# Kernel tuning notes

Hardware: AMD Instinct MI355X
Metric: run time of the kernel (lower is better)

The kernel has to match this reference:

```python
import jax, jax.numpy as jnp
import numpy as np

B, L, T = 128, 512, 25
DHID, DFRAME, DEMB, V = 1024, 512, 128, 512
DIN = DHID + DFRAME + DEMB  # 1664, LSTMCell input
EPS = 1e-5


def setup_inputs() -> dict:
    key = jax.random.key(0)
    ks = iter(jax.random.split(key, 32))
    nk = lambda: next(ks)
    rnd = lambda shape, s=0.02: jax.random.normal(nk(), shape, jnp.float32) * s
    inp = {
        "enc": jax.random.normal(nk(), (B, L, DHID), jnp.float32),
        "frames": jax.random.normal(nk(), (B, T, 512, 7, 7), jnp.float32),
        "h0": jnp.zeros((B, DHID), jnp.float32),
        "c0": jnp.zeros((B, DHID), jnp.float32),
        "max_decode": 25,
        # learned params
        "emb_w": rnd((V, DEMB), 0.1),
        "go": jax.random.uniform(nk(), (DEMB,), jnp.float32, -0.1, 0.1),
        "conv1_w": rnd((256, 512)),  # 1x1 conv == channel matmul
        "conv1_b": jnp.zeros((256,), jnp.float32),
        "bn1_g": jnp.ones((256,), jnp.float32), "bn1_b": jnp.zeros((256,), jnp.float32),
        "bn1_m": rnd((256,), 0.1), "bn1_v": jax.random.uniform(nk(), (256,), jnp.float32, 0.5, 1.5),
        "conv2_w": rnd((64, 256)),
        "conv2_b": jnp.zeros((64,), jnp.float32),
        "bn2_g": jnp.ones((64,), jnp.float32), "bn2_b": jnp.zeros((64,), jnp.float32),
        "bn2_m": rnd((64,), 0.1), "bn2_v": jax.random.uniform(nk(), (64,), jnp.float32, 0.5, 1.5),
        "fc_w": rnd((DFRAME, 64 * 7 * 7)), "fc_b": jnp.zeros((DFRAME,), jnp.float32),
        "hfc_w": rnd((DHID, DHID)), "hfc_b": jnp.zeros((DHID,), jnp.float32),
        "w_ih": rnd((4 * DHID, DIN)), "b_ih": jnp.zeros((4 * DHID,), jnp.float32),
        "w_hh": rnd((4 * DHID, DHID)), "b_hh": jnp.zeros((4 * DHID,), jnp.float32),
        "actor_w": rnd((DEMB, DHID + DIN)), "actor_b": jnp.zeros((DEMB,), jnp.float32),
    }
    return inp


def _decode(enc, frames, h0, c0, emb_w, go, conv1_w, conv1_b, bn1_g, bn1_b, bn1_m, bn1_v,
            conv2_w, conv2_b, bn2_g, bn2_b, bn2_m, bn2_v, fc_w, fc_b, hfc_w, hfc_b,
            w_ih, b_ih, w_hh, b_hh, actor_w, actor_b, max_t):
    b = enc.shape[0]
    sh = lambda p: p.reshape(1, -1, 1, 1)

    def bn(x, g, bb, m, v):  # eval-mode batchnorm, x: [B,C,7,7]
        return sh(g) * (x - sh(m)) * jax.lax.rsqrt(sh(v) + EPS) + sh(bb)

    def vis(x):  # ResnetVisualEncoder, x: [B,512,7,7]
        x = jnp.einsum('bchw,oc->bohw', x, conv1_w) + sh(conv1_b)
        x = jax.nn.relu(bn(x, bn1_g, bn1_b, bn1_m, bn1_v))
        x = jnp.einsum('bchw,oc->bohw', x, conv2_w) + sh(conv2_b)
        x = jax.nn.relu(bn(x, bn2_g, bn2_b, bn2_m, bn2_v))
        return x.reshape(b, -1) @ fc_w.T + fc_b  # [B, dframe]

    def step(carry, frame_t):
        h, c, e = carry
        vis_t = vis(frame_t)
        q = h @ hfc_w.T + hfc_b                          # h_tm1_fc
        raw = jnp.einsum('bld,bd->bl', enc, q)           # inp.bmm(h)
        score = jax.nn.softmax(raw, axis=1)              # over L
        weighted = jnp.einsum('bl,bld->bd', score, enc)  # DotAttn output
        inp = jnp.concatenate([vis_t, weighted, e], axis=1)  # [B, din]
        gates = inp @ w_ih.T + b_ih + h @ w_hh.T + b_hh
        i, f, g, o = jnp.split(gates, 4, axis=1)
        c_t = jax.nn.sigmoid(f) * c + jax.nn.sigmoid(i) * jnp.tanh(g)
        h_t = jax.nn.sigmoid(o) * jnp.tanh(c_t)
        cont = jnp.concatenate([h_t, inp], axis=1)
        action_emb = cont @ actor_w.T + actor_b
        action = action_emb @ emb_w.T                    # [B, V]
        e_t = emb_w[jnp.argmax(action, axis=1)]          # greedy feedback (eval)
        return (h_t, c_t, e_t), (action, score[..., None])

    e0 = jnp.broadcast_to(go, (b, go.shape[0]))
    frames_tbchw = jnp.swapaxes(frames[:, :max_t], 0, 1)  # [T,B,512,7,7]
    (h_t, c_t, _), (actions, scores) = jax.lax.scan(step, (h0, c0, e0), frames_tbchw)
    # out_action_high [B,T,V], out_attn_scores [B,T,L,1], state_t
    return jnp.swapaxes(actions, 0, 1), jnp.swapaxes(scores, 0, 1), h_t, c_t


def reference(enc, frames, h0, c0, max_decode, emb_w, go, conv1_w, conv1_b, bn1_g, bn1_b,
              bn1_m, bn1_v, conv2_w, conv2_b, bn2_g, bn2_b, bn2_m, bn2_v, fc_w, fc_b,
              hfc_w, hfc_b, w_ih, b_ih, w_hh, b_hh, actor_w, actor_b):
    max_t = min(int(max_decode), frames.shape[1])
    return _decode(enc, frames, h0, c0, emb_w, go, conv1_w, conv1_b, bn1_g, bn1_b, bn1_m,
                   bn1_v, conv2_w, conv2_b, bn2_g, bn2_b, bn2_m, bn2_v, fc_w, fc_b,
                   hfc_w, hfc_b, w_ih, b_ih, w_hh, b_hh, actor_w, actor_b, max_t)
```

## Files before the change

### kernel.cpp

```cpp
#include <hip/hip_runtime.h>
#include <cmath>


#define NB   128
#define NT   25
#define NL   512
#define DH   1024
#define DF   512
#define DE   128
#define DIN  1664
#define DCAT 2688
#define NV   512
#define NSEG 8
#define NGZ  6

#define ACT_OFF 0
#define SC_OFF  1638400
#define H_OFF   3276800
#define C_OFF   3407872

#define WS_W1T   0u
#define WS_W2T   131072u
#define WS_APT   147456u
#define WS_EWT   491520u
#define WS_BSUM  557056u
#define WS_A1    561152u
#define WS_B1    561408u
#define WS_A2    561664u
#define WS_B2    561728u
#define WS_XCAT  561792u
#define WS_CBUF  905856u
#define WS_QPART 1036928u
#define WS_VIS   4776576u
#define WS_Y2F   6414976u
#define WS_ATT   6414976u
#define WS_ATTRAW 7471744u
#define WS_GPART 7537280u

__global__ __launch_bounds__(256) void k_prep(
    const float* __restrict__ conv1_w, const float* __restrict__ conv1_b,
    const float* __restrict__ bn1_g, const float* __restrict__ bn1_b,
    const float* __restrict__ bn1_m, const float* __restrict__ bn1_v,
    const float* __restrict__ conv2_w, const float* __restrict__ conv2_b,
    const float* __restrict__ bn2_g, const float* __restrict__ bn2_b,
    const float* __restrict__ bn2_m, const float* __restrict__ bn2_v,
    const float* __restrict__ actor_w, const float* __restrict__ emb_w,
    const float* __restrict__ b_ih, const float* __restrict__ b_hh,
    float* __restrict__ ws)
{
  int i = blockIdx.x * 256 + threadIdx.x;
  if (i < 131072) {
    int c = i >> 8, o = i & 255;
    ws[WS_W1T + i] = conv1_w[o * 512 + c];
    return;
  }
  i -= 131072;
  if (i < 16384) {
    int c = i >> 6, o = i & 63;
    ws[WS_W2T + i] = conv2_w[o * 256 + c];
    return;
  }
  i -= 16384;
  if (i < 344064) {
    int k = i >> 7, o = i & 127;
    int src = (k < DIN) ? (DH + k) : (k - DIN);
    ws[WS_APT + i] = actor_w[o * DCAT + src];
    return;
  }
  i -= 344064;
  if (i < 65536) {
    int j = i >> 9, v = i & 511;
    ws[WS_EWT + i] = emb_w[v * 128 + j];
    return;
  }
  i -= 65536;
  if (i < 4096) { ws[WS_BSUM + i] = b_ih[i] + b_hh[i]; return; }
  i -= 4096;
  if (i < 256) {
    float a = bn1_g[i] / sqrtf(bn1_v[i] + 1e-5f);
    ws[WS_A1 + i] = a;
    ws[WS_B1 + i] = a * (conv1_b[i] - bn1_m[i]) + bn1_b[i];
    return;
  }
  i -= 256;
  if (i < 64) {
    float a = bn2_g[i] / sqrtf(bn2_v[i] + 1e-5f);
    ws[WS_A2 + i] = a;
    ws[WS_B2 + i] = a * (conv2_b[i] - bn2_m[i]) + bn2_b[i];
  }
}

__global__ __launch_bounds__(256) void k_init(
    const float* __restrict__ h0, const float* __restrict__ c0,
    const float* __restrict__ go, float* __restrict__ ws)
{
  int b = blockIdx.x, tid = threadIdx.x;
  if (tid < 128) ws[WS_XCAT + b * DCAT + 1536 + tid] = go[tid];
  for (int d = tid; d < 1024; d += 256) {
    ws[WS_XCAT + b * DCAT + 1664 + d] = h0[b * 1024 + d];
    ws[WS_CBUF + b * 1024 + d] = c0[b * 1024 + d];
  }
}

__global__ __launch_bounds__(256) void k_visconv(
    const float* __restrict__ frames, float* __restrict__ ws, int bt0)
{
  __shared__ float lds[10240];
  float* Xc  = lds;
  float* Wc  = lds + 2048;
  float* Y1c = lds;
  const int bt = bt0 + blockIdx.x, tid = threadIdx.x;
  const int tn = tid & 15, tm = tid >> 4;
  const float* img = frames + (size_t)bt * 25088;
  const float* W1T = ws + WS_W1T;
  const float* W2T = ws + WS_W2T;

  float acc1[4][16];
  #pragma unroll
  for (int m = 0; m < 4; ++m)
    #pragma unroll
    for (int j = 0; j < 16; ++j) acc1[m][j] = 0.f;

  for (int i = tid; i < 2048; i += 256) Xc[i] = 0.f;
  __syncthreads();

  for (int ch = 0; ch < 16; ++ch) {
    for (int i4 = tid; i4 < 392; i4 += 256) {
      float4 v = *(const float4*)(img + ch * 1568 + (i4 << 2));
      int gi = i4 << 2;
      #pragma unroll
      for (int j = 0; j < 4; ++j) {
        int e = gi + j, c = e / 49, hw = e - c * 49;
        Xc[(c << 6) + hw] = (&v.x)[j];
      }
    }
    const float4* wsrc = (const float4*)(W1T + (ch << 13));
    for (int i = tid; i < 2048; i += 256) ((float4*)Wc)[i] = wsrc[i];
    __syncthreads();
    #pragma unroll 4
    for (int c = 0; c < 32; ++c) {
      const float4 a4 = *(const float4*)&Xc[(c << 6) + (tm << 2)];
      float a[4] = {a4.x, a4.y, a4.z, a4.w};
      const float* wr = &Wc[(c << 8) + (tn << 2)];
      #pragma unroll
      for (int ko = 0; ko < 4; ++ko) {
        const float4 b4 = *(const float4*)&wr[ko << 6];
        float bb[4] = {b4.x, b4.y, b4.z, b4.w};
        #pragma unroll
        for (int m = 0; m < 4; ++m)
          #pragma unroll
          for (int jo = 0; jo < 4; ++jo)
            acc1[m][(ko << 2) + jo] += a[m] * bb[jo];
      }
    }
    __syncthreads();
  }

  #pragma unroll
  for (int ko = 0; ko < 4; ++ko)
    #pragma unroll
    for (int jo = 0; jo < 4; ++jo) {
      const int o = (ko << 6) + (tn << 2) + jo;
      const float aa = ws[WS_A1 + o], bb = ws[WS_B1 + o];
      #pragma unroll
      for (int m = 0; m < 4; ++m)
        acc1[m][(ko << 2) + jo] = fmaxf(aa * acc1[m][(ko << 2) + jo] + bb, 0.f);
    }

  float acc2[4][4];
  #pragma unroll
  for (int m = 0; m < 4; ++m)
    #pragma unroll
    for (int j = 0; j < 4; ++j) acc2[m][j] = 0.f;
  for (int r = 0; r < 2; ++r) {
    __syncthreads();
    #pragma unroll
    for (int kh = 0; kh < 2; ++kh) {
      const int ko = (r << 1) + kh;
      #pragma unroll
      for (int jo = 0; jo < 4; ++jo) {
        const int row = (kh << 6) + (tn << 2) + jo;
        float4 v;
        v.x = acc1[0][(ko << 2) + jo]; v.y = acc1[1][(ko << 2) + jo];
        v.z = acc1[2][(ko << 2) + jo]; v.w = acc1[3][(ko << 2) + jo];
        *(float4*)&Y1c[row * 68 + (tm << 2)] = v;
      }
    }
    __syncthreads();
    #pragma unroll 4
    for (int c2l = 0; c2l < 128; ++c2l) {
      const float4 a4 = *(const float4*)&Y1c[c2l * 68 + (tm << 2)];
      float a[4] = {a4.x, a4.y, a4.z, a4.w};
      const float4 b4 = *(const float4*)&W2T[(((r << 7) + c2l) << 6) + (tn << 2)];
      float bb[4] = {b4.x, b4.y, b4.z, b4.w};
      #pragma unroll
      for (int m = 0; m < 4; ++m)
        #pragma unroll
        for (int jo = 0; jo < 4; ++jo)
          acc2[m][jo] += a[m] * bb[jo];
    }
  }

  float* y2f = ws + WS_Y2F + (size_t)bt * 3136;
  #pragma unroll
  for (int jo = 0; jo < 4; ++jo) {
    const int o2 = (tn << 2) + jo;
    const float aa = ws[WS_A2 + o2], bb = ws[WS_B2 + o2];
    #pragma unroll
    for (int m = 0; m < 4; ++m) {
      const int hw = (tm << 2) + m;
      if (hw < 49) y2f[o2 * 49 + hw] = fmaxf(aa * acc2[m][jo] + bb, 0.f);
    }
  }
}

__global__ __launch_bounds__(256) void k_gemmfc(
    const float* __restrict__ A, const float* __restrict__ B,
    float* __restrict__ ws)
{
  __shared__ float As[32 * 68];
  __shared__ float Bs[32 * 68];
  const int tid = threadIdx.x;
  const int fid = blockIdx.x, bz = blockIdx.y;
  const int w = (fid & 7) * 50 + (fid >> 3);
  const int bm = w >> 3, bn = w & 7;
  const int tm = tid >> 4, tn = tid & 15;
  float acc[4][4];
  #pragma unroll
  for (int i = 0; i < 4; ++i)
    #pragma unroll
    for (int j = 0; j < 4; ++j) acc[i][j] = 0.f;

  const int kbase0 = bz * 1568;
  for (int kk = 0; kk < 1568; kk += 32) {
    const int kb = kbase0 + kk;
    #pragma unroll
    for (int i = 0; i < 8; ++i) {
      const int idx = tid + i * 256;
      const int mm = idx >> 5, k = idx & 31;
      As[k * 68 + mm] = A[(size_t)(bm * 64 + mm) * 3136 + kb + k];
      Bs[k * 68 + mm] = B[(size_t)(bn * 64 + mm) * 3136 + kb + k];
    }
    __syncthreads();
    #pragma unroll
    for (int k = 0; k < 32; ++k) {
      const float4 a4 = *(const float4*)&As[k * 68 + tm * 4];
      const float4 b4 = *(const float4*)&Bs[k * 68 + tn * 4];
      acc[0][0] += a4.x*b4.x; acc[0][1] += a4.x*b4.y; acc[0][2] += a4.x*b4.z; acc[0][3] += a4.x*b4.w;
      acc[1][0] += a4.y*b4.x; acc[1][1] += a4.y*b4.y; acc[1][2] += a4.y*b4.z; acc[1][3] += a4.y*b4.w;
      acc[2][0] += a4.z*b4.x; acc[2][1] += a4.z*b4.y; acc[2][2] += a4.z*b4.z; acc[2][3] += a4.z*b4.w;
      acc[3][0] += a4.w*b4.x; acc[3][1] += a4.w*b4.y; acc[3][2] += a4.w*b4.z; acc[3][3] += a4.w*b4.w;
    }
    __syncthreads();
  }
  float* Cz = ws + (bz ? WS_QPART : WS_VIS);
  #pragma unroll
  for (int i = 0; i < 4; ++i) {
    const int row = bm * 64 + tm * 4 + i;
    const int col0 = bn * 64 + tn * 4;
    float4 v;
    v.x = acc[i][0]; v.y = acc[i][1]; v.z = acc[i][2]; v.w = acc[i][3];
    *(float4*)&Cz[(size_t)row * 512 + col0] = v;
  }
}

__global__ __launch_bounds__(256) void k_fccomb(
    const float* __restrict__ fc_b, float* __restrict__ ws)
{
  const int id = blockIdx.x * 256 + threadIdx.x;
  ws[WS_VIS + id] += ws[WS_QPART + id] + fc_b[id & 511];
}

__global__ __launch_bounds__(256) void k_gemm2(
    const float* __restrict__ A, int lda,
    const float* __restrict__ B, int ldb,
    float* __restrict__ C, int ldc,
    int Kz, long strideCz)
{
  __shared__ float As[32 * 133];
  __shared__ float Bs[32 * 69];
  const int tid = threadIdx.x;
  const int bm = blockIdx.x, bn = blockIdx.y, bz = blockIdx.z;
  const int tm = tid >> 4, tn = tid & 15;
  float acc[8][4];
  #pragma unroll
  for (int i = 0; i < 8; ++i)
    #pragma unroll
    for (int j = 0; j < 4; ++j) acc[i][j] = 0.f;

  const int kbase0 = bz * Kz;
  for (int kk = 0; kk < Kz; kk += 32) {
    const int kb = kbase0 + kk;
    #pragma unroll
    for (int i = 0; i < 16; ++i) {
      const int e = tid + i * 256;
      const int k = e & 31, m = e >> 5;
      As[k * 133 + m] = A[(size_t)(bm * 128 + m) * lda + kb + k];
    }
    #pragma unroll
    for (int i = 0; i < 8; ++i) {
      const int e = tid + i * 256;
      const int k = e & 31, n = e >> 5;
      Bs[k * 69 + n] = B[(size_t)(bn * 64 + n) * ldb + kb + k];
    }
    __syncthreads();
    #pragma unroll
    for (int k = 0; k < 32; ++k) {
      const float4 a0 = *(const float4*)&As[k * 133 + tm * 8];
      const float4 a1 = *(const float4*)&As[k * 133 + tm * 8 + 4];
      const float4 b4 = *(const float4*)&Bs[k * 69 + tn * 4];
      const float av[8] = {a0.x, a0.y, a0.z, a0.w, a1.x, a1.y, a1.z, a1.w};
      const float bv[4] = {b4.x, b4.y, b4.z, b4.w};
      #pragma unroll
      for (int i = 0; i < 8; ++i)
        #pragma unroll
        for (int j = 0; j < 4; ++j)
          acc[i][j] += av[i] * bv[j];
    }
    __syncthreads();
  }
  float* Cz = C + (long)bz * strideCz;
  #pragma unroll
  for (int i = 0; i < 8; ++i) {
    const int row = bm * 128 + tm * 8 + i;
    const int col0 = bn * 64 + tn * 4;
    float4 v;
    v.x = acc[i][0]; v.y = acc[i][1]; v.z = acc[i][2]; v.w = acc[i][3];
    *(float4*)&Cz[(size_t)row * ldc + col0] = v;
  }
}

__global__ __launch_bounds__(512) void k_attn(
    const float* __restrict__ enc, const float* __restrict__ hfc_b,
    float* __restrict__ ws)
{
  __shared__ float q_lds[1024];
  __shared__ float raw_lds[64];
  __shared__ float accw[8][1024];
  __shared__ float m_lds[8];
  __shared__ float z_lds[8];
  const int seg = blockIdx.x, b = blockIdx.y, tid = threadIdx.x;
  const float* qpart = ws + WS_QPART;
  for (int d = tid; d < 1024; d += 512) {
    float s = hfc_b[d];
    #pragma unroll
    for (int sp = 0; sp < 8; ++sp) s += qpart[sp * 131072 + b * 1024 + d];
    q_lds[d] = s;
  }
  __syncthreads();
  const int lane = tid & 63, wv = tid >> 6;
  const float4 q0 = *(const float4*)&q_lds[lane * 4];
  const float4 q1 = *(const float4*)&q_lds[lane * 4 + 256];
  const float4 q2 = *(const float4*)&q_lds[lane * 4 + 512];
  const float4 q3 = *(const float4*)&q_lds[lane * 4 + 768];
  const float* row = enc + (size_t)b * (NL * DH) + (size_t)seg * 64 * DH + lane * 4;
  float m = -INFINITY, z = 0.f;
  float4 ac0 = {0,0,0,0}, ac1 = {0,0,0,0}, ac2 = {0,0,0,0}, ac3 = {0,0,0,0};
  float4 e0 = *(const float4*)&row[wv * 1024];
  float4 e1 = *(const float4*)&row[wv * 1024 + 256];
  float4 e2 = *(const float4*)&row[wv * 1024 + 512];
  float4 e3 = *(const float4*)&row[wv * 1024 + 768];
  for (int r = 0; r < 8; ++r) {
    const int l = wv + (r << 3);
    const float4 c0_ = e0, c1_ = e1, c2_ = e2, c3_ = e3;
    if (r < 7) {
      const int ln = (l + 8) * 1024;
      e0 = *(const float4*)&row[ln];
      e1 = *(const float4*)&row[ln + 256];
      e2 = *(const float4*)&row[ln + 512];
      e3 = *(const float4*)&row[ln + 768];
    }
    float d = c0_.x*q0.x + c0_.y*q0.y + c0_.z*q0.z + c0_.w*q0.w;
    d += c1_.x*q1.x + c1_.y*q1.y + c1_.z*q1.z + c1_.w*q1.w;
    d += c2_.x*q2.x + c2_.y*q2.y + c2_.z*q2.z + c2_.w*q2.w;
    d += c3_.x*q3.x + c3_.y*q3.y + c3_.z*q3.z + c3_.w*q3.w;
    #pragma unroll
    for (int off = 32; off > 0; off >>= 1) d += __shfl_xor(d, off, 64);
    if (lane == 0) raw_lds[l] = d;
    const float mn = fmaxf(m, d);
    const float sc = expf(m - mn);
    const float p  = expf(d - mn);
    z = z * sc + p;
    ac0.x = ac0.x*sc + p*c0_.x; ac0.y = ac0.y*sc + p*c0_.y; ac0.z = ac0.z*sc + p*c0_.z; ac0.w = ac0.w*sc + p*c0_.w;
    ac1.x = ac1.x*sc + p*c1_.x; ac1.y = ac1.y*sc + p*c1_.y; ac1.z = ac1.z*sc + p*c1_.z; ac1.w = ac1.w*sc + p*c1_.w;
    ac2.x = ac2.x*sc + p*c2_.x; ac2.y = ac2.y*sc + p*c2_.y; ac2.z = ac2.z*sc + p*c2_.z; ac2.w = ac2.w*sc + p*c2_.w;
    ac3.x = ac3.x*sc + p*c3_.x; ac3.y = ac3.y*sc + p*c3_.y; ac3.z = ac3.z*sc + p*c3_.z; ac3.w = ac3.w*sc + p*c3_.w;
    m = mn;
  }
  *(float4*)&accw[wv][lane * 4      ] = ac0;
  *(float4*)&accw[wv][lane * 4 + 256] = ac1;
  *(float4*)&accw[wv][lane * 4 + 512] = ac2;
  *(float4*)&accw[wv][lane * 4 + 768] = ac3;
  if (lane == 0) { m_lds[wv] = m; z_lds[wv] = z; }
  __syncthreads();
  float M = m_lds[0];
  #pragma unroll
  for (int s = 1; s < 8; ++s) M = fmaxf(M, m_lds[s]);
  float ef[8];
  #pragma unroll
  for (int s = 0; s < 8; ++s) ef[s] = expf(m_lds[s] - M);
  float Z = 0.f;
  #pragma unroll
  for (int s = 0; s < 8; ++s) Z += ef[s] * z_lds[s];
  float* att = ws + WS_ATT + ((size_t)b * NSEG + seg) * 1032;
  for (int d = tid; d < 1024; d += 512) {
    float s = 0.f;
    #pragma unroll
    for (int w8 = 0; w8 < 8; ++w8) s += ef[w8] * accw[w8][d];
    att[d] = s;
  }
  if (tid == 0) { att[1024] = M; att[1025] = Z; }
  if (tid < 64) ws[WS_ATTRAW + b * 512 + seg * 64 + tid] = raw_lds[tid];
}

__global__ __launch_bounds__(256) void k_comb(
    float* __restrict__ ws, float* __restrict__ out, int t)
{
  const int b = blockIdx.x, tid = threadIdx.x;
  const float* att = ws + WS_ATT + (size_t)b * NSEG * 1032;
  float* xcat = ws + WS_XCAT + (size_t)b * DCAT;
  float ms[NSEG], zs[NSEG];
  #pragma unroll
  for (int s = 0; s < NSEG; ++s) { ms[s] = att[s * 1032 + 1024]; zs[s] = att[s * 1032 + 1025]; }
  float M = ms[0];
  #pragma unroll
  for (int s = 1; s < NSEG; ++s) M = fmaxf(M, ms[s]);
  float ef[NSEG], Z = 0.f;
  #pragma unroll
  for (int s = 0; s < NSEG; ++s) { ef[s] = expf(ms[s] - M); Z += ef[s] * zs[s]; }
  const float inv = 1.f / Z;
  for (int i = tid; i < 512; i += 256)
    xcat[i] = ws[WS_VIS + ((size_t)b * NT + t) * DF + i];
  for (int d = tid; d < 1024; d += 256) {
    float w = 0.f;
    #pragma unroll
    for (int s = 0; s < NSEG; ++s) w += ef[s] * att[s * 1032 + d];
    xcat[512 + d] = w * inv;
  }
  for (int l = tid; l < 512; l += 256)
    out[SC_OFF + ((size_t)b * NT + t) * NL + l] =
        expf(ws[WS_ATTRAW + b * 512 + l] - M) * inv;
}

__global__ __launch_bounds__(256) void k_gates(
    const float* __restrict__ w_ih, const float* __restrict__ w_hh,
    float* __restrict__ ws)
{
  __shared__ float As[32 * 68];
  __shared__ float Bs[32 * 68];
  const int tid = threadIdx.x;
  const int bm = blockIdx.x, bn = blockIdx.y, bz = blockIdx.z;
  const int tm = tid >> 4, tn = tid & 15;
  float acc[4][4];
  #pragma unroll
  for (int i = 0; i < 4; ++i)
    #pragma unroll
    for (int j = 0; j < 4; ++j) acc[i][j] = 0.f;

  const float* xc = ws + WS_XCAT;
  for (int kk = 0; kk < 448; kk += 32) {
    const int kb = bz * 448 + kk;
    #pragma unroll
    for (int i = 0; i < 2; ++i) {
      const int e = tid + i * 256;
      const int r = e >> 3, kq = e & 7;
      const float4 av = *(const float4*)&xc[(size_t)(bm * 64 + r) * DCAT + kb + kq * 4];
      As[(kq * 4 + 0) * 68 + r] = av.x;
      As[(kq * 4 + 1) * 68 + r] = av.y;
      As[(kq * 4 + 2) * 68 + r] = av.z;
      As[(kq * 4 + 3) * 68 + r] = av.w;
      const int g = bn * 64 + r;
      const float4 bv = (kb < DIN)
          ? *(const float4*)&w_ih[(size_t)g * DIN + kb + kq * 4]
          : *(const float4*)&w_hh[(size_t)g * DH + (kb - DIN) + kq * 4];
      Bs[(kq * 4 + 0) * 68 + r] = bv.x;
      Bs[(kq * 4 + 1) * 68 + r] = bv.y;
      Bs[(kq * 4 + 2) * 68 + r] = bv.z;
      Bs[(kq * 4 + 3) * 68 + r] = bv.w;
    }
    __syncthreads();
    #pragma unroll
    for (int k = 0; k < 32; ++k) {
      const float4 a4 = *(const float4*)&As[k * 68 + tm * 4];
      const float4 b4 = *(const float4*)&Bs[k * 68 + tn * 4];
      acc[0][0] += a4.x*b4.x; acc[0][1] += a4.x*b4.y; acc[0][2] += a4.x*b4.z; acc[0][3] += a4.x*b4.w;
      acc[1][0] += a4.y*b4.x; acc[1][1] += a4.y*b4.y; acc[1][2] += a4.y*b4.z; acc[1][3] += a4.y*b4.w;
      acc[2][0] += a4.z*b4.x; acc[2][1] += a4.z*b4.y; acc[2][2] += a4.z*b4.z; acc[2][3] += a4.z*b4.w;
      acc[3][0] += a4.w*b4.x; acc[3][1] += a4.w*b4.y; acc[3][2] += a4.w*b4.z; acc[3][3] += a4.w*b4.w;
    }
    __syncthreads();
  }
  float* Cz = ws + WS_GPART + (size_t)bz * 524288;
  #pragma unroll
  for (int i = 0; i < 4; ++i) {
    const int b = bm * 64 + tm * 4 + i;
    const int col0 = bn * 64 + tn * 4;
    float4 v;
    v.x = acc[i][0]; v.y = acc[i][1]; v.z = acc[i][2]; v.w = acc[i][3];
    *(float4*)&Cz[(size_t)b * 4096 + col0] = v;
  }
}

__global__ __launch_bounds__(512) void k_lstmactor(
    const float* __restrict__ emb_w, const float* __restrict__ actor_b,
    float* __restrict__ ws, float* __restrict__ out, int t, int last)
{
  __shared__ float xl[DCAT];
  __shared__ float ph[512];
  __shared__ float ae[128];
  __shared__ float bv[512];
  __shared__ int   bi[512];
  const int b = blockIdx.x, tid = threadIdx.x;
  float* xcat = ws + WS_XCAT + (size_t)b * DCAT;

  for (int i = tid; i < 416; i += 512)
    ((float4*)xl)[i] = ((const float4*)xcat)[i];

  const float* gpart = ws + WS_GPART;
  const float* bsum = ws + WS_BSUM;
  for (int j = tid; j < 1024; j += 512) {
    float g[4];
    #pragma unroll
    for (int gi = 0; gi < 4; ++gi) {
      const int x = gi * 1024 + j;
      float s = bsum[x];
      #pragma unroll
      for (int sp = 0; sp < NGZ; ++sp) s += gpart[(size_t)sp * 524288 + b * 4096 + x];
      g[gi] = s;
    }
    const float ii = 1.f / (1.f + expf(-g[0]));
    const float ff = 1.f / (1.f + expf(-g[1]));
    const float gg = tanhf(g[2]);
    const float oo = 1.f / (1.f + expf(-g[3]));
    const float c = ff * ws[WS_CBUF + b * 1024 + j] + ii * gg;
    const float h = oo * tanhf(c);
    ws[WS_CBUF + b * 1024 + j] = c;
    xl[1664 + j] = h;
    xcat[1664 + j] = h;
    if (last) { out[H_OFF + b * 1024 + j] = h; out[C_OFF + b * 1024 + j] = c; }
  }
  __syncthreads();

  {
    const int o = tid & 127;
    const int k0 = (tid >> 7) * 672;
    const float* APT = ws + WS_APT;
    float s = 0.f;
    #pragma unroll 8
    for (int k = k0; k < k0 + 672; ++k) s += xl[k] * APT[k * 128 + o];
    ph[tid] = s;
  }
  __syncthreads();
  if (tid < 128)
    ae[tid] = ph[tid] + ph[tid + 128] + ph[tid + 256] + ph[tid + 384] + actor_b[tid];
  __syncthreads();

  const float* EWT = ws + WS_EWT;
  float s = 0.f;
  #pragma unroll 8
  for (int j = 0; j < 128; ++j) s += ae[j] * EWT[j * 512 + tid];
  out[ACT_OFF + ((size_t)b * NT + t) * NV + tid] = s;
  bv[tid] = s; bi[tid] = tid;
  __syncthreads();
  for (int s2 = 256; s2 > 0; s2 >>= 1) {
    if (tid < s2) {
      float ov = bv[tid + s2]; int oi = bi[tid + s2];
      if (ov > bv[tid] || (ov == bv[tid] && oi < bi[tid])) { bv[tid] = ov; bi[tid] = oi; }
    }
    __syncthreads();
  }
  const int am = bi[0];
  if (tid < 128) xcat[1536 + tid] = emb_w[am * 128 + tid];
}

extern "C" void kernel_launch(void* const* d_in, const int* in_sizes, int n_in,
                              void* d_out, int out_size, void* d_ws, size_t ws_size,
                              hipStream_t stream)
{
  const float* enc     = (const float*)d_in[0];
  const float* frames  = (const float*)d_in[1];
  const float* h0      = (const float*)d_in[2];
  const float* c0      = (const float*)d_in[3];
  const float* emb_w   = (const float*)d_in[5];
  const float* go      = (const float*)d_in[6];
  const float* conv1_w = (const float*)d_in[7];
  const float* conv1_b = (const float*)d_in[8];
  const float* bn1_g   = (const float*)d_in[9];
  const float* bn1_b   = (const float*)d_in[10];
  const float* bn1_m   = (const float*)d_in[11];
  const float* bn1_v   = (const float*)d_in[12];
  const float* conv2_w = (const float*)d_in[13];
  const float* conv2_b = (const float*)d_in[14];
  const float* bn2_g   = (const float*)d_in[15];
  const float* bn2_b   = (const float*)d_in[16];
  const float* bn2_m   = (const float*)d_in[17];
  const float* bn2_v   = (const float*)d_in[18];
  const float* fc_w    = (const float*)d_in[19];
  const float* fc_b    = (const float*)d_in[20];
  const float* hfc_w   = (const float*)d_in[21];
  const float* hfc_b   = (const float*)d_in[22];
  const float* w_ih    = (const float*)d_in[23];
  const float* b_ih    = (const float*)d_in[24];
  const float* w_hh    = (const float*)d_in[25];
  const float* b_hh    = (const float*)d_in[26];
  const float* actor_w = (const float*)d_in[27];
  const float* actor_b = (const float*)d_in[28];
  float* out = (float*)d_out;
  float* ws  = (float*)d_ws;

  k_prep<<<2194, 256, 0, stream>>>(conv1_w, conv1_b, bn1_g, bn1_b, bn1_m, bn1_v,
      conv2_w, conv2_b, bn2_g, bn2_b, bn2_m, bn2_v, actor_w, emb_w, b_ih, b_hh, ws);
  k_init<<<128, 256, 0, stream>>>(h0, c0, go, ws);
  for (int c = 0; c < 16; ++c)
    k_visconv<<<200, 256, 0, stream>>>(frames, ws, c * 200);
  k_gemmfc<<<dim3(400, 2), 256, 0, stream>>>(ws + WS_Y2F, fc_w, ws);
  k_fccomb<<<6400, 256, 0, stream>>>(fc_b, ws);

  for (int t = 0; t < NT; ++t) {
    k_gemm2<<<dim3(1, 16, 8), 256, 0, stream>>>(ws + WS_XCAT + 1664, DCAT,
        hfc_w, 1024, ws + WS_QPART, 1024, 128, 131072);
    k_attn<<<dim3(NSEG, 128), 512, 0, stream>>>(enc, hfc_b, ws);
    k_comb<<<128, 256, 0, stream>>>(ws, out, t);
    k_gates<<<dim3(2, 64, 6), 256, 0, stream>>>(w_ih, w_hh, ws);
    k_lstmactor<<<128, 512, 0, stream>>>(emb_w, actor_b, ws, out, t,
                                         t == NT - 1 ? 1 : 0);
  }
}
```

Baseline: 6.541 ms.

## Cover full batch per gates block and double split-K in LSTM gate GEMM

The LSTM gate GEMM now gives each block all 128 batch rows with an 8x4 per-thread micro-tile, instead of splitting the batch across two blocks. Each weight tile of w_ih/w_hh is therefore streamed from memory once rather than twice. To keep the same number of blocks, split-K goes from 6 to 12, which doubles the partial-sum writes and the reduction reads in the consumer kernel. It also needs a larger partial workspace and more registers per thread.

Result: no change. 6.588 ms (+0.7%).

```diff
diff --git a/kernel.cpp b/kernel.cpp
--- a/kernel.cpp
+++ b/kernel.cpp
@@ -12,7 +12,7 @@
 #define DCAT 2688
 #define NV   512
 #define NSEG 8
-#define NGZ  6
+#define NGZ  12
 
 #define ACT_OFF 0
 #define SC_OFF  1638400
@@ -446,54 +446,63 @@
     const float* __restrict__ w_ih, const float* __restrict__ w_hh,
     float* __restrict__ ws)
 {
-  __shared__ float As[32 * 68];
+  __shared__ float As[32 * 132];
   __shared__ float Bs[32 * 68];
   const int tid = threadIdx.x;
-  const int bm = blockIdx.x, bn = blockIdx.y, bz = blockIdx.z;
+  const int bn = blockIdx.x, bz = blockIdx.y;
   const int tm = tid >> 4, tn = tid & 15;
-  float acc[4][4];
-  #pragma unroll
-  for (int i = 0; i < 4; ++i)
+  float acc[8][4];
+  #pragma unroll
+  for (int i = 0; i < 8; ++i)
     #pragma unroll
     for (int j = 0; j < 4; ++j) acc[i][j] = 0.f;
 
   const float* xc = ws + WS_XCAT;
-  for (int kk = 0; kk < 448; kk += 32) {
-    const int kb = bz * 448 + kk;
+  for (int kk = 0; kk < 224; kk += 32) {
+    const int kb = bz * 224 + kk;
+    #pragma unroll
+    for (int i = 0; i < 4; ++i) {
+      const int e = tid + i * 256;
+      const int r = e >> 3, kq = e & 7;
+      const float4 av = *(const float4*)&xc[(size_t)r * DCAT + kb + kq * 4];
+      As[(kq * 4 + 0) * 132 + r] = av.x;
+      As[(kq * 4 + 1) * 132 + r] = av.y;
+      As[(kq * 4 + 2) * 132 + r] = av.z;
+      As[(kq * 4 + 3) * 132 + r] = av.w;
+    }
     #pragma unroll
     for (int i = 0; i < 2; ++i) {
       const int e = tid + i * 256;
-      const int r = e >> 3, kq = e & 7;
-      const float4 av = *(const float4*)&xc[(size_t)(bm * 64 + r) * DCAT + kb + kq * 4];
-      As[(kq * 4 + 0) * 68 + r] = av.x;
-      As[(kq * 4 + 1) * 68 + r] = av.y;
-      As[(kq * 4 + 2) * 68 + r] = av.z;
-      As[(kq * 4 + 3) * 68 + r] = av.w;
-      const int g = bn * 64 + r;
+      const int n = e >> 3, kq = e & 7;
+      const int g = bn * 64 + n;
       const float4 bv = (kb < DIN)
           ? *(const float4*)&w_ih[(size_t)g * DIN + kb + kq * 4]
           : *(const float4*)&w_hh[(size_t)g * DH + (kb - DIN) + kq * 4];
-      Bs[(kq * 4 + 0) * 68 + r] = bv.x;
-      Bs[(kq * 4 + 1) * 68 + r] = bv.y;
-      Bs[(kq * 4 + 2) * 68 + r] = bv.z;
-      Bs[(kq * 4 + 3) * 68 + r] = bv.w;
+      Bs[(kq * 4 + 0) * 68 + n] = bv.x;
+      Bs[(kq * 4 + 1) * 68 + n] = bv.y;
+      Bs[(kq * 4 + 2) * 68 + n] = bv.z;
+      Bs[(kq * 4 + 3) * 68 + n] = bv.w;
     }
     __syncthreads();
     #pragma unroll
     for (int k = 0; k < 32; ++k) {
-      const float4 a4 = *(const float4*)&As[k * 68 + tm * 4];
+      const float4 a0 = *(const float4*)&As[k * 132 + tm * 8];
+      const float4 a1 = *(const float4*)&As[k * 132 + tm * 8 + 4];
       const float4 b4 = *(const float4*)&Bs[k * 68 + tn * 4];
-      acc[0][0] += a4.x*b4.x; acc[0][1] += a4.x*b4.y; acc[0][2] += a4.x*b4.z; acc[0][3] += a4.x*b4.w;
-      acc[1][0] += a4.y*b4.x; acc[1][1] += a4.y*b4.y; acc[1][2] += a4.y*b4.z; acc[1][3] += a4.y*b4.w;
-      acc[2][0] += a4.z*b4.x; acc[2][1] += a4.z*b4.y; acc[2][2] += a4.z*b4.z; acc[2][3] += a4.z*b4.w;
-      acc[3][0] += a4.w*b4.x; acc[3][1] += a4.w*b4.y; acc[3][2] += a4.w*b4.z; acc[3][3] += a4.w*b4.w;
+      const float av[8] = {a0.x, a0.y, a0.z, a0.w, a1.x, a1.y, a1.z, a1.w};
+      const float bv[4] = {b4.x, b4.y, b4.z, b4.w};
+      #pragma unroll
+      for (int i = 0; i < 8; ++i)
+        #pragma unroll
+        for (int j = 0; j < 4; ++j)
+          acc[i][j] += av[i] * bv[j];
     }
     __syncthreads();
   }
   float* Cz = ws + WS_GPART + (size_t)bz * 524288;
   #pragma unroll
-  for (int i = 0; i < 4; ++i) {
-    const int b = bm * 64 + tm * 4 + i;
+  for (int i = 0; i < 8; ++i) {
+    const int b = tm * 8 + i;
     const int col0 = bn * 64 + tn * 4;
     float4 v;
     v.x = acc[i][0]; v.y = acc[i][1]; v.z = acc[i][2]; v.w = acc[i][3];
@@ -621,7 +630,7 @@
         hfc_w, 1024, ws + WS_QPART, 1024, 128, 131072);
     k_attn<<<dim3(NSEG, 128), 512, 0, stream>>>(enc, hfc_b, ws);
     k_comb<<<128, 256, 0, stream>>>(ws, out, t);
-    k_gates<<<dim3(2, 64, 6), 256, 0, stream>>>(w_ih, w_hh, ws);
+    k_gates<<<dim3(64, NGZ), 256, 0, stream>>>(w_ih, w_hh, ws);
     k_lstmactor<<<128, 512, 0, stream>>>(emb_w, actor_b, ws, out, t,
                                          t == NT - 1 ? 1 : 0);
   }
```
